# Optimization experiments

Hardware: AMD Instinct MI355X
Metric: run time of the kernel (lower is better)

The kernel has to match this reference:

```python
import jax, jax.numpy as jnp
import numpy as np
import math

D_MODEL = 512
N_HEADS = 8
D_FF = 2048
TOP_FACTOR = 5
LN_EPS = 1e-5


def _layernorm(x, g, b):
    m = jnp.mean(x, axis=-1, keepdims=True)
    v = jnp.mean((x - m) ** 2, axis=-1, keepdims=True)
    return (x - m) / jnp.sqrt(v + LN_EPS) * g + b


def _prob_sparse_attn(q_in, k_in, v_in, wq, bq, wk, bk, wv, bv, wo, bo):
    # weights stored (in, out): y = x @ w + b  (equivalent to torch Linear)
    B, Lq, dm = q_in.shape
    Lk = k_in.shape[1]
    H, D = N_HEADS, dm // N_HEADS
    q = (q_in @ wq + bq).reshape(B, Lq, H, D).transpose(0, 2, 1, 3)  # (B,H,Lq,D)
    k = (k_in @ wk + bk).reshape(B, Lk, H, D).transpose(0, 2, 1, 3)
    v = (v_in @ wv + bv).reshape(B, Lk, H, D).transpose(0, 2, 1, 3)

    qn = q / jnp.linalg.norm(q, axis=-1, keepdims=True)
    kn = k / jnp.linalg.norm(k, axis=-1, keepdims=True)
    # full cosine-similarity matrix, reduced to a row mean (as in the original)
    scores_all = jnp.einsum('bhqd,bhkd->bhqk', qn, kn)
    mean_scores = scores_all.mean(axis=-1)  # (B,H,Lq)

    u = max(1, Lq // TOP_FACTOR)
    _, top_idx = jax.lax.top_k(mean_scores, u)  # (B,H,u)

    q_sel = jnp.take_along_axis(q, top_idx[..., None], axis=2)  # (B,H,u,D)
    scores = jnp.einsum('bhud,bhkd->bhuk', q_sel, k) / math.sqrt(D)
    attn = jax.nn.softmax(scores, axis=-1)
    ctx_sel = jnp.einsum('bhuk,bhkd->bhud', attn, v)  # (B,H,u,D)

    b_ix = jnp.arange(B)[:, None, None]
    h_ix = jnp.arange(H)[None, :, None]
    context = jnp.zeros((B, H, Lq, D), dtype=q.dtype).at[b_ix, h_ix, top_idx].set(ctx_sel)
    out = context.transpose(0, 2, 1, 3).reshape(B, Lq, dm)
    return out @ wo + bo


def _decoder_layer(x, enc_out, p):
    xn = _layernorm(x, p['ln1_g'], p['ln1_b'])
    x = x + _prob_sparse_attn(xn, xn, xn, p['sa_wq'], p['sa_bq'], p['sa_wk'], p['sa_bk'],
                              p['sa_wv'], p['sa_bv'], p['sa_wo'], p['sa_bo'])
    xn = _layernorm(x, p['ln2_g'], p['ln2_b'])
    x = x + _prob_sparse_attn(xn, enc_out, enc_out, p['ca_wq'], p['ca_bq'], p['ca_wk'], p['ca_bk'],
                              p['ca_wv'], p['ca_bv'], p['ca_wo'], p['ca_bo'])
    xn = _layernorm(x, p['ln3_g'], p['ln3_b'])
    h = jax.nn.relu(xn @ p['ff_w1'] + p['ff_b1'])
    return x + (h @ p['ff_w2'] + p['ff_b2'])


def setup_inputs() -> dict:
    key = jax.random.key(0)
    ks = iter(jax.random.split(key, 32))
    B, L = 2, 2048
    dm, dff = D_MODEL, D_FF
    s = 1.0 / math.sqrt(dm)
    inp = {
        'x': jax.random.normal(next(ks), (B, L, dm), jnp.float32),
        'enc_out': jax.random.normal(next(ks), (B, L, dm), jnp.float32),
    }
    for pre in ('sa', 'ca'):
        for nm in ('wq', 'wk', 'wv', 'wo'):
            inp[f'{pre}_{nm}'] = jax.random.normal(next(ks), (dm, dm), jnp.float32) * s
            inp[f'{pre}_{nm[1:] and "b" + nm[1:]}'] = jnp.zeros((dm,), jnp.float32)
    inp['ff_w1'] = jax.random.normal(next(ks), (dm, dff), jnp.float32) * s
    inp['ff_b1'] = jnp.zeros((dff,), jnp.float32)
    inp['ff_w2'] = jax.random.normal(next(ks), (dff, dm), jnp.float32) / math.sqrt(dff)
    inp['ff_b2'] = jnp.zeros((dm,), jnp.float32)
    for i in (1, 2, 3):
        inp[f'ln{i}_g'] = jnp.ones((dm,), jnp.float32)
        inp[f'ln{i}_b'] = jnp.zeros((dm,), jnp.float32)
    return inp


def reference(x, enc_out,
              sa_wq, sa_bq, sa_wk, sa_bk, sa_wv, sa_bv, sa_wo, sa_bo,
              ca_wq, ca_bq, ca_wk, ca_bk, ca_wv, ca_bv, ca_wo, ca_bo,
              ff_w1, ff_b1, ff_w2, ff_b2,
              ln1_g, ln1_b, ln2_g, ln2_b, ln3_g, ln3_b):
    p = dict(sa_wq=sa_wq, sa_bq=sa_bq, sa_wk=sa_wk, sa_bk=sa_bk, sa_wv=sa_wv, sa_bv=sa_bv,
             sa_wo=sa_wo, sa_bo=sa_bo, ca_wq=ca_wq, ca_bq=ca_bq, ca_wk=ca_wk, ca_bk=ca_bk,
             ca_wv=ca_wv, ca_bv=ca_bv, ca_wo=ca_wo, ca_bo=ca_bo,
             ff_w1=ff_w1, ff_b1=ff_b1, ff_w2=ff_w2, ff_b2=ff_b2,
             ln1_g=ln1_g, ln1_b=ln1_b, ln2_g=ln2_g, ln2_b=ln2_b, ln3_g=ln3_g, ln3_b=ln3_b)
    return _decoder_layer(x, enc_out, p)
```

## Files before the change

### kernel.cpp

```cpp
#include <hip/hip_runtime.h>

#define BB 2
#define LL 2048
#define DM 512
#define NH 8
#define DH 64
#define DFF 2048
#define UU 409
#define ROWS (BB*LL)
#define X_ELEMS 2097152
#define NCHUNK 8

typedef unsigned short u16;
typedef __attribute__((ext_vector_type(8))) short short8;
typedef __attribute__((ext_vector_type(4))) float floatx4;

#define G_TOTAL 38200000
__device__ float g_buf[G_TOTAL];
__device__ int   g_isbf16;

#define A_Q     10495488
#define A_K     12592640
#define A_V     14689792
#define A_MKN   25175552
#define A_MS    25176576
#define A_RANK  25209344
#define A_PARTK 25242112
#define A_LIST  25274880
#define A_PO    25281536
#define A_PML   29475840
#define A_CTXF  16786944
#define XN_H    16796672
#define XN_L    18893824
#define CTX_H   33573888
#define CTX_L   35671040
#define ENC_H   37768192
#define ENC_L   39865344
#define AH_H    41962496
#define KH16    59213824
#define KL16    61310976
#define VTH16   63408128
#define VTL16   65505280
#define WT_SAQKV 67864576
#define WT_SAO   69437440
#define WT_CAQ   69961728
#define WT_CAKV  70486016
#define WT_CAO   71534592
#define WT_W1    72058880
#define WT_W2    74156032

__constant__ int c_end[28] = {
    2097152, 4194304, 4456448, 4456960, 4719104, 4719616, 4981760, 4982272,
    5244416, 5244928, 5507072, 5507584, 5769728, 5770240, 6032384, 6032896,
    6295040, 6295552, 7344128, 7346176, 8394752, 8395264, 8395776, 8396288,
    8396800, 8397312, 8397824, 8398336
};
__constant__ int sm_idx[16] = {3,5,7,9,11,13,15,17,19,21,22,23,24,25,26,27};
__constant__ int sm_cum[16] = {64,128,192,256,320,384,448,512,768,832,896,960,1024,1088,1152,1216};
#define XG 262144
#define EG 262144
#define SG 1216

__device__ __forceinline__ float bf2f(u16 x) {
    union { unsigned int u; float f; } c; c.u = ((unsigned int)x) << 16; return c.f;
}
__device__ __forceinline__ u16 f2bf(float f) {
    union { float f; unsigned int u; } c; c.f = f;
    unsigned int u = c.u;
    return (u16)((u + 0x7FFFu + ((u >> 16) & 1u)) >> 16);
}
__device__ __forceinline__ unsigned cvtpk_bf16(float a, float b) {
    unsigned r;
    asm("v_cvt_pk_bf16_f32 %0, %1, %2" : "=v"(r) : "v"(a), "v"(b));
    return r;
}

struct P28 { const void* p[28]; };
struct I3 { int v[3]; };

__constant__ int tj[10][6] = {
    {2,  WT_SAQKV, 0,    512,  786432, 8},
    {4,  WT_SAQKV, 512,  512,  786432, 8},
    {6,  WT_SAQKV, 1024, 512,  786432, 8},
    {8,  WT_SAO,   0,    512,  262144, 8},
    {10, WT_CAQ,   0,    512,  262144, 8},
    {12, WT_CAKV,  0,    512,  524288, 8},
    {14, WT_CAKV,  512,  512,  524288, 8},
    {16, WT_CAO,   0,    512,  262144, 8},
    {18, WT_W1,    0,    512, 1048576, 32},
    {20, WT_W2,    0,   2048, 1048576, 8},
};
__constant__ int tcum[10] = {64, 128, 192, 256, 320, 384, 448, 512, 768, 1024};
__global__ void prep_all(P28 ps) {
    const int f = (((const u16*)ps.p[22])[0] == 0x3F80u) ? 1 : 0;
    if (blockIdx.x == 0 && threadIdx.x == 0) g_isbf16 = f;
    u16* gb16 = (u16*)g_buf;
    if (blockIdx.x < 1024) {
        int bid = blockIdx.x;
        int j = 0;
        while (bid >= tcum[j]) j++;
        int t = bid - (j ? tcum[j - 1] : 0);
        int widx = tj[j][0], wt = tj[j][1], col0 = tj[j][2];
        int K = tj[j][3], lo = tj[j][4], txn = tj[j][5];
        int Nsrc = txn * 64;
        int n0 = (t % txn) * 64, k0 = (t / txn) * 64;
        __shared__ float tb[64][65];
        int c = threadIdx.x & 63, r0 = threadIdx.x >> 6;
        const void* W = ps.p[widx];
        u16* WTh = gb16 + wt;
        for (int i = 0; i < 16; i++) {
            int r = r0 + 4 * i;
            size_t src = (size_t)(k0 + r) * Nsrc + n0 + c;
            tb[r][c] = f ? bf2f(((const u16*)W)[src]) : ((const float*)W)[src];
        }
        __syncthreads();
        for (int i = 0; i < 16; i++) {
            int r = r0 + 4 * i;
            float v = tb[c][r];
            u16 hi = f2bf(v);
            size_t o = (size_t)(col0 + n0 + r) * K + k0 + c;
            WTh[o] = hi;
            WTh[lo + o] = f2bf(v - bf2f(hi));
        }
        return;
    }
    int stride = 2048 * blockDim.x;
    for (int g = (blockIdx.x - 1024) * blockDim.x + threadIdx.x; g < XG + EG + SG; g += stride) {
        if (g < XG) {
            int e = g * 8;
            if (f) {
                uint4 raw = ((const uint4*)ps.p[0])[g];
                const u16* rr = (const u16*)&raw;
                float v[8] __attribute__((aligned(16)));
#pragma unroll
                for (int i = 0; i < 8; i++) v[i] = bf2f(rr[i]);
                *(float4*)(g_buf + e) = ((const float4*)v)[0];
                *(float4*)(g_buf + e + 4) = ((const float4*)v)[1];
            } else {
                *(uint4*)(g_buf + e)     = ((const uint4*)ps.p[0])[g * 2];
                *(uint4*)(g_buf + e + 4) = ((const uint4*)ps.p[0])[g * 2 + 1];
            }
        } else if (g < XG + EG) {
            int gl = g - XG;
            int e = gl * 8;
            float v[8] __attribute__((aligned(16)));
            if (f) {
                uint4 raw = ((const uint4*)ps.p[1])[gl];
                const u16* rr = (const u16*)&raw;
#pragma unroll
                for (int i = 0; i < 8; i++) v[i] = bf2f(rr[i]);
            } else {
                *(float4*)(v)     = ((const float4*)ps.p[1])[gl * 2];
                *(float4*)(v + 4) = ((const float4*)ps.p[1])[gl * 2 + 1];
            }
            u16 hh[8] __attribute__((aligned(16)));
            u16 lo[8] __attribute__((aligned(16)));
#pragma unroll
            for (int i = 0; i < 8; i++) { u16 hi = f2bf(v[i]); hh[i] = hi; lo[i] = f2bf(v[i] - bf2f(hi)); }
            *(uint4*)(&gb16[ENC_H + e]) = *(const uint4*)hh;
            *(uint4*)(&gb16[ENC_L + e]) = *(const uint4*)lo;
        } else {
            int t = g - XG - EG;
            int si = 0;
            while (t >= sm_cum[si]) si++;
            int s = sm_idx[si];
            int gl = t - (si ? sm_cum[si - 1] : 0);
            int e = gl * 8;
            float* dst = g_buf + c_end[s - 1] + e;
            if (f) {
                uint4 raw = *(const uint4*)((const u16*)ps.p[s] + e);
                const u16* rr = (const u16*)&raw;
#pragma unroll
                for (int i = 0; i < 8; i++) dst[i] = bf2f(rr[i]);
            } else {
                *(uint4*)(dst)     = *(const uint4*)((const float*)ps.p[s] + e);
                *(uint4*)(dst + 4) = *(const uint4*)((const float*)ps.p[s] + e + 4);
            }
        }
    }
}

__global__ void lnorm_k(int x_off, int g_off, int b_off, int yh_u16, int yl_u16) {
    int row = blockIdx.x;
    int tid = threadIdx.x;
    const float* x = g_buf + x_off + (size_t)row * DM;
    float a = x[tid], c = x[tid + 256];
    float s1 = a + c, s2 = a * a + c * c;
    for (int o = 32; o > 0; o >>= 1) { s1 += __shfl_xor(s1, o); s2 += __shfl_xor(s2, o); }
    __shared__ float r1[4], r2[4];
    int wave = tid >> 6, lane = tid & 63;
    if (lane == 0) { r1[wave] = s1; r2[wave] = s2; }
    __syncthreads();
    s1 = r1[0] + r1[1] + r1[2] + r1[3];
    s2 = r2[0] + r2[1] + r2[2] + r2[3];
    float mean = s1 * (1.0f / DM);
    float var  = s2 * (1.0f / DM) - mean * mean;
    float rstd = rsqrtf(var + 1e-5f);
    const float* gg = g_buf + g_off;
    const float* bb = g_buf + b_off;
    u16* yh = ((u16*)g_buf) + yh_u16 + (size_t)row * DM;
    u16* yl = ((u16*)g_buf) + yl_u16 + (size_t)row * DM;
    float v1 = (a - mean) * rstd * gg[tid]       + bb[tid];
    float v2 = (c - mean) * rstd * gg[tid + 256] + bb[tid + 256];
    u16 h1 = f2bf(v1), h2 = f2bf(v2);
    yh[tid] = h1;       yl[tid] = f2bf(v1 - bf2f(h1));
    yh[tid + 256] = h2; yl[tid + 256] = f2bf(v2 - bf2f(h2));
}

template<int WM, bool SPLIT, bool SEC, bool RELU, bool RESID, bool FINAL, bool OUTH>
__global__ void mgemm_k(I3 a_offs, I3 splt, I3 alz, int wt_u16_off, I3 boffs, int resid_off,
                        int out_off, void* __restrict__ dext, int M, int N, int K) {
    constexpr int BT_M = WM * 32;
    constexpr int A4 = BT_M * 4;
    __shared__ u16 Ash[BT_M * 40];
    __shared__ u16 Asl[SPLIT ? BT_M * 40 : 8];
    __shared__ u16 Bsh[128 * 40];
    __shared__ u16 Bsl[SPLIT ? 128 * 40 : 8];
    int sec_blk = SEC ? ((blockIdx.x * 128) >> 9) : 0;
    const u16* Ah = ((const u16*)g_buf) + a_offs.v[sec_blk];
    const u16* Al = Ah + (size_t)M * K;
    const u16* WTh = ((const u16*)g_buf) + wt_u16_off;
    const u16* WTl = WTh + (size_t)N * K;
    const int isbf = g_isbf16;
    const bool use_al = SPLIT && splt.v[sec_blk] && !(alz.v[sec_blk] && isbf);
    const bool use_bl = SPLIT && splt.v[sec_blk] && !isbf;
    int tid = threadIdx.x;
    int lane = tid & 63, wid = tid >> 6;
    int wm = wid >> 1, wn = wid & 1;
    int quad = lane >> 4, l15 = lane & 15;
    int m0 = blockIdx.y * BT_M, n0 = blockIdx.x * 128;
    floatx4 acc[WM][4];
#pragma unroll
    for (int i = 0; i < WM; i++)
#pragma unroll
        for (int j = 0; j < 4; j++) acc[i][j] = (floatx4){0.f, 0.f, 0.f, 0.f};
    for (int k0 = 0; k0 < K; k0 += 32) {
#pragma unroll
        for (int i = 0; i < (A4 + 255) / 256; i++) {
            int idx8 = tid + 256 * i;
            if (A4 % 256 == 0 || idx8 < A4) {
                int r = idx8 >> 2, c8 = (idx8 & 3) * 8;
                *(uint4*)(&Ash[r * 40 + c8]) = *(const uint4*)(Ah + (size_t)(m0 + r) * K + k0 + c8);
                if (SPLIT && use_al)
                    *(uint4*)(&Asl[r * 40 + c8]) = *(const uint4*)(Al + (size_t)(m0 + r) * K + k0 + c8);
            }
        }
#pragma unroll
        for (int i = 0; i < 2; i++) {
            int idx8 = tid + 256 * i;
            int r = idx8 >> 2, c8 = (idx8 & 3) * 8;
            *(uint4*)(&Bsh[r * 40 + c8]) = *(const uint4*)(WTh + (size_t)(n0 + r) * K + k0 + c8);
            if (SPLIT && use_bl)
                *(uint4*)(&Bsl[r * 40 + c8]) = *(const uint4*)(WTl + (size_t)(n0 + r) * K + k0 + c8);
        }
        __syncthreads();
        short8 ah[WM], bh[4], al[WM], bl[4];
#pragma unroll
        for (int i = 0; i < WM; i++) {
            int ro = (wm * WM * 16 + i * 16 + l15) * 40 + quad * 8;
            ah[i] = *(const short8*)(&Ash[ro]);
            if (SPLIT && use_al) al[i] = *(const short8*)(&Asl[ro]);
        }
#pragma unroll
        for (int j = 0; j < 4; j++) {
            int ro = (wn * 64 + j * 16 + l15) * 40 + quad * 8;
            bh[j] = *(const short8*)(&Bsh[ro]);
            if (SPLIT && use_bl) bl[j] = *(const short8*)(&Bsl[ro]);
        }
#pragma unroll
        for (int i = 0; i < WM; i++)
#pragma unroll
            for (int j = 0; j < 4; j++) {
                acc[i][j] = __builtin_amdgcn_mfma_f32_16x16x32_bf16(ah[i], bh[j], acc[i][j], 0, 0, 0);
                if constexpr (SPLIT) {
                    if (use_bl)
                        acc[i][j] = __builtin_amdgcn_mfma_f32_16x16x32_bf16(ah[i], bl[j], acc[i][j], 0, 0, 0);
                    if (use_al)
                        acc[i][j] = __builtin_amdgcn_mfma_f32_16x16x32_bf16(al[i], bh[j], acc[i][j], 0, 0, 0);
                }
            }
        __syncthreads();
    }
#pragma unroll
    for (int i = 0; i < WM; i++)
#pragma unroll
        for (int j = 0; j < 4; j++)
#pragma unroll
            for (int r = 0; r < 4; r++) {
                int row = m0 + wm * WM * 16 + i * 16 + quad * 4 + r;
                int col = n0 + wn * 64 + j * 16 + l15;
                int sec = SEC ? (col >> 9) : 0;
                int ci  = SEC ? (col & 511) : col;
                float v = acc[i][j][r] + g_buf[boffs.v[sec] + ci];
                if (RELU) v = fmaxf(v, 0.f);
                if (RESID) v += g_buf[resid_off + (size_t)row * N + col];
                if (FINAL) {
                    if (g_isbf16) ((u16*)dext)[(size_t)row * N + col] = f2bf(v);
                    else          ((float*)dext)[(size_t)row * N + col] = v;
                } else if (OUTH) {
                    ((u16*)g_buf)[out_off + (size_t)row * N + col] = f2bf(v);
                } else if (SEC) {
                    g_buf[out_off + ((size_t)sec * ROWS + row) * 512 + ci] = v;
                } else {
                    g_buf[out_off + (size_t)row * N + col] = v;
                }
            }
}

template<bool SPLIT, bool RESID, bool FINAL>
__global__ __launch_bounds__(64, 2) void sgemm_k(int a_off, int sp, int alz, int wt_u16_off,
        int b_off, int resid_off, int out_off, void* __restrict__ dext, int M, int N, int K) {
    const u16* gb = (const u16*)g_buf;
    const u16* Ah = gb + a_off;
    const u16* Alp = Ah + (size_t)M * K;
    const u16* Bh = gb + wt_u16_off;
    const u16* Blp = Bh + (size_t)N * K;
    const int isbf = g_isbf16;
    const bool ual = SPLIT && sp && !(alz && isbf);
    const bool ubl = SPLIT && sp && !isbf;
    int ntiles = N >> 6;
    int bid = blockIdx.x;
    int nt = bid % ntiles, mt = bid / ntiles;
    int n0 = nt * 64, m0 = mt * 16;
    int lane = threadIdx.x;
    int quad = lane >> 4, l15 = lane & 15;
    const u16* ap  = Ah  + (size_t)(m0 + l15) * K + quad * 8;
    const u16* alq = Alp + (size_t)(m0 + l15) * K + quad * 8;
    const u16* bp  = Bh  + (size_t)(n0 + l15) * K + quad * 8;
    const u16* blq = Blp + (size_t)(n0 + l15) * K + quad * 8;
    floatx4 acc[4];
#pragma unroll
    for (int j = 0; j < 4; j++) acc[j] = (floatx4){0.f, 0.f, 0.f, 0.f};
#pragma unroll 2
    for (int k0 = 0; k0 < K; k0 += 32) {
        short8 ah = *(const short8*)(ap + k0);
        short8 al;
        if (ual) al = *(const short8*)(alq + k0);
        short8 bh[4], bl[4];
#pragma unroll
        for (int j = 0; j < 4; j++) {
            bh[j] = *(const short8*)(bp + (size_t)j * 16 * K + k0);
            if (ubl) bl[j] = *(const short8*)(blq + (size_t)j * 16 * K + k0);
        }
#pragma unroll
        for (int j = 0; j < 4; j++) {
            acc[j] = __builtin_amdgcn_mfma_f32_16x16x32_bf16(ah, bh[j], acc[j], 0, 0, 0);
            if constexpr (SPLIT) {
                if (ubl) acc[j] = __builtin_amdgcn_mfma_f32_16x16x32_bf16(ah, bl[j], acc[j], 0, 0, 0);
                if (ual) acc[j] = __builtin_amdgcn_mfma_f32_16x16x32_bf16(al, bh[j], acc[j], 0, 0, 0);
            }
        }
    }
    const float* bias = g_buf + b_off;
#pragma unroll
    for (int j = 0; j < 4; j++)
#pragma unroll
        for (int r = 0; r < 4; r++) {
            int row = m0 + quad * 4 + r;
            int col = n0 + j * 16 + l15;
            float v = acc[j][r] + bias[col];
            if (RESID) v += g_buf[resid_off + (size_t)row * N + col];
            if (FINAL) {
                if (isbf) ((u16*)dext)[(size_t)row * N + col] = f2bf(v);
                else      ((float*)dext)[(size_t)row * N + col] = v;
            } else {
                g_buf[out_off + (size_t)row * N + col] = v;
            }
        }
}

__global__ void meankn_p1(int k_off, int part_off) {
    int bh = blockIdx.x >> 5, chunk = blockIdx.x & 31;
    int b = bh >> 3, h = bh & 7;
    int wave = threadIdx.x >> 6, lane = threadIdx.x & 63;
    const float* base = g_buf + k_off + (size_t)b * LL * DM + (size_t)h * DH + lane;
    float acc = 0.f;
    for (int t = 0; t < 16; t++) {
        int j = chunk * 64 + wave * 16 + t;
        float kv = base[(size_t)j * DM];
        float s = kv * kv;
        for (int o = 32; o > 0; o >>= 1) s += __shfl_xor(s, o);
        acc += kv / sqrtf(fmaxf(s, 1e-30f));
    }
    __shared__ float red[4][64];
    red[wave][lane] = acc;
    __syncthreads();
    if (threadIdx.x < 64)
        g_buf[part_off + (size_t)blockIdx.x * 64 + threadIdx.x] =
            red[0][threadIdx.x] + red[1][threadIdx.x] + red[2][threadIdx.x] + red[3][threadIdx.x];
}

__global__ void mscore_k(int q_off, int part_off, int ms_off) {
    int bh = blockIdx.y, b = bh >> 3, h = bh & 7;
    int tid = threadIdx.x;
    __shared__ float mk[64];
    if (tid < 64) {
        float s = 0.f;
        for (int c = 0; c < 32; c++) s += g_buf[part_off + (size_t)(bh * 32 + c) * 64 + tid];
        mk[tid] = s * (1.0f / LL);
    }
    __syncthreads();
    int w = tid >> 6, lane = tid & 63;
    float m = mk[lane];
#pragma unroll
    for (int it = 0; it < 8; it++) {
        int row = blockIdx.x * 32 + it * 4 + w;
        float qv = g_buf[q_off + ((size_t)b * LL + row) * DM + h * DH + lane];
        float s = qv * qv, d = qv * m;
        for (int o = 32; o > 0; o >>= 1) { s += __shfl_xor(s, o); d += __shfl_xor(d, o); }
        if (lane == 0) g_buf[ms_off + bh * LL + row] = d / sqrtf(fmaxf(s, 1e-30f));
    }
}

__global__ void topsel_k(int ms_off, int list_off, int rank_off, int u) {
    __shared__ float s[LL];
    int bh = blockIdx.y, chunk = blockIdx.x;
    for (int i = threadIdx.x; i < LL; i += 256) s[i] = g_buf[ms_off + bh * LL + i];
    __syncthreads();
    int il = threadIdx.x >> 2;
    int i = chunk * 64 + il;
    int jq = threadIdx.x & 3;
    float si = s[i];
    int cnt = 0;
    for (int t = 0; t < 512; t++) {
        int j = jq * 512 + t;
        float sj = s[j];
        cnt += (sj > si) || (sj == si && j < i);
    }
    cnt += __shfl_xor(cnt, 1);
    cnt += __shfl_xor(cnt, 2);
    if (jq == 0) {
        int* list = (int*)(g_buf + list_off);
        int* rank = (int*)(g_buf + rank_off);
        if (cnt < u) { list[bh * 416 + cnt] = i; rank[bh * LL + i] = cnt; }
        else rank[bh * LL + i] = -1;
    }
}

template<bool LO>
__global__ void kvprep_k(int k_off, int v_off) {
    int bh = blockIdx.y, b = bh >> 3, h = bh & 7;
    int tok0 = blockIdx.x * 64;
    int tid = threadIdx.x;
    __shared__ float vt[64][68];
    u16* gb16 = (u16*)g_buf;
    int tok = tid >> 2, dq = (tid & 3) * 16;
    const float* kp = g_buf + k_off + ((size_t)(b * LL + tok0 + tok)) * DM + h * DH + dq;
    const float* vp = g_buf + v_off + ((size_t)(b * LL + tok0 + tok)) * DM + h * DH + dq;
    float kv[16] __attribute__((aligned(16)));
#pragma unroll
    for (int i = 0; i < 4; i++) *(float4*)(kv + 4 * i) = *(const float4*)(kp + 4 * i);
    u16 hh[16] __attribute__((aligned(16)));
    u16 lo[16] __attribute__((aligned(16)));
#pragma unroll
    for (int i = 0; i < 16; i++) { hh[i] = f2bf(kv[i]); if (LO) lo[i] = f2bf(kv[i] - bf2f(hh[i])); }
    size_t ko = ((size_t)(bh * LL + tok0 + tok)) * DH + dq;
    *(uint4*)(gb16 + KH16 + ko)     = ((const uint4*)hh)[0];
    *(uint4*)(gb16 + KH16 + ko + 8) = ((const uint4*)hh)[1];
    if (LO) {
        *(uint4*)(gb16 + KL16 + ko)     = ((const uint4*)lo)[0];
        *(uint4*)(gb16 + KL16 + ko + 8) = ((const uint4*)lo)[1];
    }
#pragma unroll
    for (int i = 0; i < 4; i++) *(float4*)(&vt[tok][dq + 4 * i]) = *(const float4*)(vp + 4 * i);
    __syncthreads();
    int d = tid >> 2, tq = (tid & 3) * 16;
    float vv[16];
#pragma unroll
    for (int i = 0; i < 16; i++) vv[i] = vt[tq + i][d];
#pragma unroll
    for (int i = 0; i < 16; i++) { hh[i] = f2bf(vv[i]); if (LO) lo[i] = f2bf(vv[i] - bf2f(hh[i])); }
    size_t vo = ((size_t)(bh * DH + d)) * LL + tok0 + tq;
    *(uint4*)(gb16 + VTH16 + vo)     = ((const uint4*)hh)[0];
    *(uint4*)(gb16 + VTH16 + vo + 8) = ((const uint4*)hh)[1];
    if (LO) {
        *(uint4*)(gb16 + VTL16 + vo)     = ((const uint4*)lo)[0];
        *(uint4*)(gb16 + VTL16 + vo + 8) = ((const uint4*)lo)[1];
    }
}

template<bool S3>
__global__ __launch_bounds__(256, 4) void attn_flash(int q_off, int kh_off, int kl_off,
        int vth_off, int vtl_off, int list_off, int po_off, int pml_off, int u) {
    int bid = blockIdx.x;
    int grp = bid & 127;
    int sxt = bid >> 7;
    int bh = grp & 15, chunk = grp >> 4;
    int b = bh >> 3, h = bh & 7;
    int tid = threadIdx.x, lane = tid & 63, w = tid >> 6;
    int quad = lane >> 4, l15 = lane & 15;
    const int* list = (const int*)(g_buf + list_off);

    short8 qh[2], ql[2];
    {
        int slot_q = sxt * 64 + w * 16 + l15;
        int qidx = list[bh * 416 + (slot_q < u ? slot_q : u - 1)];
        const float* qp = g_buf + q_off + ((size_t)b * LL + qidx) * DM + h * DH;
#pragma unroll
        for (int d2 = 0; d2 < 2; d2++) {
            float v[8] __attribute__((aligned(16)));
            *(float4*)(v)     = *(const float4*)(qp + d2 * 32 + quad * 8);
            *(float4*)(v + 4) = *(const float4*)(qp + d2 * 32 + quad * 8 + 4);
            u16 hh[8] __attribute__((aligned(16)));
            u16 lo[8] __attribute__((aligned(16)));
#pragma unroll
            for (int j = 0; j < 8; j++) {
                float s = v[j] * 0.125f;
                u16 hi = f2bf(s); hh[j] = hi; lo[j] = f2bf(s - bf2f(hi));
            }
            qh[d2] = *(const short8*)hh; ql[d2] = *(const short8*)lo;
        }
    }

    __shared__ u16 Ksh[32 * 68];
    __shared__ u16 Ksl[S3 ? 32 * 68 : 8];
    __shared__ u16 Vth[64 * 36];
    __shared__ u16 Vtl[S3 ? 64 * 36 : 8];

    const u16* gb16 = (const u16*)g_buf;
    const u16* KHp = gb16 + kh_off + (size_t)bh * LL * DH;
    const u16* KLp = gb16 + kl_off + (size_t)bh * LL * DH;
    const u16* VHp = gb16 + vth_off + (size_t)bh * DH * LL;
    const u16* VLp = gb16 + vtl_off + (size_t)bh * DH * LL;
    int krow = tid >> 3, kcol = (tid & 7) * 8;
    int vd = tid >> 2, vcol = (tid & 3) * 8;

    int aA = ((((lane >> 4) & 1) << 5) | l15) << 2;
    int aB = aA + 64;
    bool hiT = (quad >= 2);

    uint4 pre[S3 ? 4 : 2];
    auto issue = [&](int row0) {
        pre[0] = *(const uint4*)(KHp + (size_t)(row0 + krow) * DH + kcol);
        pre[1] = *(const uint4*)(VHp + (size_t)vd * LL + row0 + vcol);
        if constexpr (S3) {
            pre[2] = *(const uint4*)(KLp + (size_t)(row0 + krow) * DH + kcol);
            pre[3] = *(const uint4*)(VLp + (size_t)vd * LL + row0 + vcol);
        }
    };
    auto commit = [&]() {
        *(uint4*)(&Ksh[krow * 68 + kcol]) = pre[0];
        *(uint4*)(&Vth[vd * 36 + vcol]) = pre[1];
        if constexpr (S3) {
            *(uint4*)(&Ksl[krow * 68 + kcol]) = pre[2];
            *(uint4*)(&Vtl[vd * 36 + vcol]) = pre[3];
        }
    };

    float m_run = -3.0e38f, l_run = 0.f;
    floatx4 acc_o[4];
#pragma unroll
    for (int j = 0; j < 4; j++) acc_o[j] = (floatx4){0.f, 0.f, 0.f, 0.f};

    issue(chunk * 256);
    for (int kt = 0; kt < 8; ++kt) {
        __syncthreads();
        commit();
        if (kt < 7) issue(chunk * 256 + (kt + 1) * 32);
        __syncthreads();
        floatx4 sacc[2];
#pragma unroll
        for (int t = 0; t < 2; t++) {
            sacc[t] = (floatx4){0.f, 0.f, 0.f, 0.f};
#pragma unroll
            for (int d2 = 0; d2 < 2; d2++) {
                int ro = (t * 16 + l15) * 68 + d2 * 32 + quad * 8;
                short8 kh = *(const short8*)(&Ksh[ro]);
                sacc[t] = __builtin_amdgcn_mfma_f32_16x16x32_bf16(kh, qh[d2], sacc[t], 0, 0, 0);
                sacc[t] = __builtin_amdgcn_mfma_f32_16x16x32_bf16(kh, ql[d2], sacc[t], 0, 0, 0);
                if constexpr (S3) {
                    short8 kl = *(const short8*)(&Ksl[ro]);
                    sacc[t] = __builtin_amdgcn_mfma_f32_16x16x32_bf16(kl, qh[d2], sacc[t], 0, 0, 0);
                }
            }
        }
        float mx = fmaxf(fmaxf(fmaxf(sacc[0][0], sacc[0][1]), fmaxf(sacc[0][2], sacc[0][3])),
                         fmaxf(fmaxf(sacc[1][0], sacc[1][1]), fmaxf(sacc[1][2], sacc[1][3])));
        mx = fmaxf(mx, __shfl_xor(mx, 16));
        mx = fmaxf(mx, __shfl_xor(mx, 32));
        float mn = fmaxf(m_run, mx);
        float alpha = __expf(m_run - mn);
        m_run = mn;
#pragma unroll
        for (int t = 0; t < 2; t++)
#pragma unroll
            for (int r = 0; r < 4; r++) sacc[t][r] = __expf(sacc[t][r] - mn);
        float ls = (sacc[0][0] + sacc[0][1]) + (sacc[0][2] + sacc[0][3])
                 + (sacc[1][0] + sacc[1][1]) + (sacc[1][2] + sacc[1][3]);
        ls += __shfl_xor(ls, 16);
        ls += __shfl_xor(ls, 32);
        l_run = l_run * alpha + ls;
        unsigned phw[2][2], plw[2][2];
#pragma unroll
        for (int t = 0; t < 2; t++)
#pragma unroll
            for (int hh = 0; hh < 2; hh++) {
                float s0 = sacc[t][2 * hh], s1 = sacc[t][2 * hh + 1];
                unsigned hw = cvtpk_bf16(s0, s1);
                phw[t][hh] = hw;
                float r0 = s0 - __uint_as_float(hw << 16);
                float r1 = s1 - __uint_as_float(hw & 0xFFFF0000u);
                plw[t][hh] = cvtpk_bf16(r0, r1);
            }
        union { unsigned wd[4]; short8 v; } pbh, pbl;
#pragma unroll
        for (int hh = 0; hh < 2; hh++) {
            int a0 = __builtin_amdgcn_ds_bpermute(aA, (int)phw[0][hh]);
            int a1 = __builtin_amdgcn_ds_bpermute(aA, (int)phw[1][hh]);
            pbh.wd[hh] = (unsigned)(hiT ? a1 : a0);
            int b0 = __builtin_amdgcn_ds_bpermute(aB, (int)phw[0][hh]);
            int b1 = __builtin_amdgcn_ds_bpermute(aB, (int)phw[1][hh]);
            pbh.wd[2 + hh] = (unsigned)(hiT ? b1 : b0);
            int c0 = __builtin_amdgcn_ds_bpermute(aA, (int)plw[0][hh]);
            int c1 = __builtin_amdgcn_ds_bpermute(aA, (int)plw[1][hh]);
            pbl.wd[hh] = (unsigned)(hiT ? c1 : c0);
            int d0 = __builtin_amdgcn_ds_bpermute(aB, (int)plw[0][hh]);
            int d1 = __builtin_amdgcn_ds_bpermute(aB, (int)plw[1][hh]);
            pbl.wd[2 + hh] = (unsigned)(hiT ? d1 : d0);
        }
#pragma unroll
        for (int j = 0; j < 4; j++)
#pragma unroll
            for (int r = 0; r < 4; r++) acc_o[j][r] *= alpha;
#pragma unroll
        for (int j = 0; j < 4; j++) {
            int ro = (j * 16 + l15) * 36 + quad * 8;
            short8 vh = *(const short8*)(&Vth[ro]);
            acc_o[j] = __builtin_amdgcn_mfma_f32_16x16x32_bf16(vh, pbh.v, acc_o[j], 0, 0, 0);
            acc_o[j] = __builtin_amdgcn_mfma_f32_16x16x32_bf16(vh, pbl.v, acc_o[j], 0, 0, 0);
            if constexpr (S3) {
                short8 vl = *(const short8*)(&Vtl[ro]);
                acc_o[j] = __builtin_amdgcn_mfma_f32_16x16x32_bf16(vl, pbh.v, acc_o[j], 0, 0, 0);
            }
        }
    }
    int slot = sxt * 64 + w * 16 + l15;
    if (slot < u) {
        size_t rec = ((size_t)(bh * NCHUNK + chunk)) * 512 + slot;
        float* po = g_buf + po_off + rec * 64;
#pragma unroll
        for (int j = 0; j < 4; j++)
            *(float4*)(po + j * 16 + quad * 4) = *(const float4*)&acc_o[j];
        if (quad == 0) {
            float* pml = g_buf + pml_off + rec * 2;
            pml[0] = m_run; pml[1] = l_run;
        }
    }
}

__global__ void attn_combine(int po_off, int pml_off, int rank_off, int u) {
    int bh = blockIdx.y;
    int b = bh >> 3, h = bh & 7;
    int tid = threadIdx.x;
    int qi = tid >> 4;
    int kb = tid & 15;
    int ds = kb * 4;
    int row = blockIdx.x * 16 + qi;
    int rank = ((const int*)(g_buf + rank_off))[bh * LL + row];
    size_t idx = ((size_t)b * LL + row) * DM + h * DH + ds;
    if (rank < 0) {
        ushort4 z = {0, 0, 0, 0};
        *(ushort4*)(((u16*)g_buf) + CTX_H + idx) = z;
        *(ushort4*)(((u16*)g_buf) + CTX_L + idx) = z;
        return;
    }
    float m = -3.0e38f;
#pragma unroll
    for (int c = 0; c < NCHUNK; c++)
        m = fmaxf(m, g_buf[pml_off + (((size_t)(bh * NCHUNK + c)) * 512 + rank) * 2]);
    float l = 0.f, O0 = 0.f, O1 = 0.f, O2 = 0.f, O3 = 0.f;
#pragma unroll
    for (int c = 0; c < NCHUNK; c++) {
        size_t rec = ((size_t)(bh * NCHUNK + c)) * 512 + rank;
        const float* pml = g_buf + pml_off + rec * 2;
        float a = __expf(pml[0] - m);
        l += a * pml[1];
        float4 o = *(const float4*)(g_buf + po_off + rec * 64 + ds);
        O0 += a * o.x; O1 += a * o.y; O2 += a * o.z; O3 += a * o.w;
    }
    float inv = 1.0f / l;
    float o0 = O0 * inv, o1 = O1 * inv, o2 = O2 * inv, o3 = O3 * inv;
    ushort4 hv, lv;
    hv.x = f2bf(o0); lv.x = f2bf(o0 - bf2f(hv.x));
    hv.y = f2bf(o1); lv.y = f2bf(o1 - bf2f(hv.y));
    hv.z = f2bf(o2); lv.z = f2bf(o2 - bf2f(hv.z));
    hv.w = f2bf(o3); lv.w = f2bf(o3 - bf2f(hv.w));
    *(ushort4*)(((u16*)g_buf) + CTX_H + idx) = hv;
    *(ushort4*)(((u16*)g_buf) + CTX_L + idx) = lv;
}

extern "C" void kernel_launch(void* const* d_in, const int* in_sizes, int n_in,
                              void* d_out, int out_size, void* d_ws, size_t ws_size,
                              hipStream_t stream) {
    static const int SZ[28] = {
        2097152, 2097152,
        262144, 512, 262144, 512, 262144, 512, 262144, 512,
        262144, 512, 262144, 512, 262144, 512, 262144, 512,
        1048576, 2048, 1048576, 512,
        512, 512, 512, 512, 512, 512
    };
    int OFF[28];
    int cur = 0;
    for (int i = 0; i < 28; i++) { OFF[i] = cur; cur += SZ[i]; }

    P28 ps;
    for (int i = 0; i < 28; i++) ps.p[i] = d_in[i];
    prep_all<<<3072, 256, 0, stream>>>(ps);

    auto select_attend = [&](bool sa) {
        if (sa) kvprep_k<true><<<dim3(32, 16), 256, 0, stream>>>(A_K, A_V);
        else    kvprep_k<false><<<dim3(32, 16), 256, 0, stream>>>(A_K, A_V);
        meankn_p1<<<16 * 32, 256, 0, stream>>>(A_K, A_PARTK);
        mscore_k<<<dim3(64, 16), 256, 0, stream>>>(A_Q, A_PARTK, A_MS);
        topsel_k<<<dim3(32, 16), 256, 0, stream>>>(A_MS, A_LIST, A_RANK, UU);
        if (sa)
            attn_flash<true><<<896, 256, 0, stream>>>(
                A_Q, KH16, KL16, VTH16, VTL16, A_LIST, A_PO, A_PML, UU);
        else
            attn_flash<false><<<896, 256, 0, stream>>>(
                A_Q, KH16, KL16, VTH16, VTL16, A_LIST, A_PO, A_PML, UU);
        attn_combine<<<dim3(128, 16), 256, 0, stream>>>(A_PO, A_PML, A_RANK, UU);
    };

    lnorm_k<<<ROWS, 256, 0, stream>>>(OFF[0], OFF[22], OFF[23], XN_H, XN_L);
    mgemm_k<2, true, true, false, false, false, false><<<dim3(12, 64), 256, 0, stream>>>(
        I3{{XN_H, XN_H, XN_H}}, I3{{1, 1, 1}}, I3{{0, 0, 0}},
        WT_SAQKV, I3{{OFF[3], OFF[5], OFF[7]}}, 0, A_Q, nullptr, ROWS, 1536, 512);
    select_attend(true);
    sgemm_k<true, true, false><<<2048, 64, 0, stream>>>(
        CTX_H, 1, 0, WT_SAO, OFF[9], OFF[0], OFF[0], nullptr, ROWS, 512, 512);

    lnorm_k<<<ROWS, 256, 0, stream>>>(OFF[0], OFF[24], OFF[25], XN_H, XN_L);
    sgemm_k<true, false, false><<<2048, 64, 0, stream>>>(
        XN_H, 1, 0, WT_CAQ, OFF[11], 0, A_Q, nullptr, ROWS, 512, 512);
    mgemm_k<2, true, true, false, false, false, false><<<dim3(8, 64), 256, 0, stream>>>(
        I3{{ENC_H, ENC_H, ENC_H}}, I3{{1, 0, 0}}, I3{{1, 0, 0}},
        WT_CAKV, I3{{OFF[13], OFF[15], 0}}, 0, A_K, nullptr, ROWS, 1024, 512);
    select_attend(false);
    sgemm_k<false, true, false><<<2048, 64, 0, stream>>>(
        CTX_H, 0, 0, WT_CAO, OFF[17], OFF[0], OFF[0], nullptr, ROWS, 512, 512);

    lnorm_k<<<ROWS, 256, 0, stream>>>(OFF[0], OFF[26], OFF[27], XN_H, XN_L);
    mgemm_k<4, false, false, true, false, false, true><<<dim3(16, 32), 256, 0, stream>>>(
        I3{{XN_H, 0, 0}}, I3{{0, 0, 0}}, I3{{0, 0, 0}},
        WT_W1, I3{{OFF[19], 0, 0}}, 0, AH_H, nullptr, ROWS, 2048, 512);
    sgemm_k<false, true, true><<<2048, 64, 0, stream>>>(
        AH_H, 0, 0, WT_W2, OFF[21], OFF[0], 0, d_out, ROWS, 512, 2048);
}
```

Baseline: 623.2 us.

## Prefetch next k-slice in sgemm and swap block order to M-fastest in GEMMs

The skinny GEMM kernel now double-buffers its register fragments, loading the next k-step's A/B fragments before issuing the MFMAs for the current one, so global-load latency can overlap with compute. It also drops the min-blocks-per-CU launch bound, which gives the compiler more registers for the extra buffers. Both GEMM kernels switch block rasterization so consecutive blocks walk M with a fixed N tile, aiming for better weight-tile reuse in cache. The costs are higher register pressure and possibly fewer waves resident per CU.

```diff
diff --git a/kernel.cpp b/kernel.cpp
--- a/kernel.cpp
+++ b/kernel.cpp
@@ -216,7 +216,8 @@
     __shared__ u16 Asl[SPLIT ? BT_M * 40 : 8];
     __shared__ u16 Bsh[128 * 40];
     __shared__ u16 Bsl[SPLIT ? 128 * 40 : 8];
-    int sec_blk = SEC ? ((blockIdx.x * 128) >> 9) : 0;
+    int ntb = blockIdx.y;
+    int sec_blk = SEC ? ((ntb * 128) >> 9) : 0;
     const u16* Ah = ((const u16*)g_buf) + a_offs.v[sec_blk];
     const u16* Al = Ah + (size_t)M * K;
     const u16* WTh = ((const u16*)g_buf) + wt_u16_off;
@@ -228,7 +229,7 @@
     int lane = tid & 63, wid = tid >> 6;
     int wm = wid >> 1, wn = wid & 1;
     int quad = lane >> 4, l15 = lane & 15;
-    int m0 = blockIdx.y * BT_M, n0 = blockIdx.x * 128;
+    int m0 = blockIdx.x * BT_M, n0 = ntb * 128;
     floatx4 acc[WM][4];
 #pragma unroll
     for (int i = 0; i < WM; i++)
@@ -308,7 +309,7 @@
 }
 
 template<bool SPLIT, bool RESID, bool FINAL>
-__global__ __launch_bounds__(64, 2) void sgemm_k(int a_off, int sp, int alz, int wt_u16_off,
+__global__ __launch_bounds__(64) void sgemm_k(int a_off, int sp, int alz, int wt_u16_off,
         int b_off, int resid_off, int out_off, void* __restrict__ dext, int M, int N, int K) {
     const u16* gb = (const u16*)g_buf;
     const u16* Ah = gb + a_off;
@@ -318,9 +319,9 @@
     const int isbf = g_isbf16;
     const bool ual = SPLIT && sp && !(alz && isbf);
     const bool ubl = SPLIT && sp && !isbf;
-    int ntiles = N >> 6;
+    int mtiles = M >> 4;
     int bid = blockIdx.x;
-    int nt = bid % ntiles, mt = bid / ntiles;
+    int mt = bid % mtiles, nt = bid / mtiles;
     int n0 = nt * 64, m0 = mt * 16;
     int lane = threadIdx.x;
     int quad = lane >> 4, l15 = lane & 15;
@@ -331,24 +332,40 @@
     floatx4 acc[4];
 #pragma unroll
     for (int j = 0; j < 4; j++) acc[j] = (floatx4){0.f, 0.f, 0.f, 0.f};
-#pragma unroll 2
+    short8 ah_c, al_c, bh_c[4], bl_c[4];
+    ah_c = *(const short8*)(ap);
+    if (ual) al_c = *(const short8*)(alq);
+#pragma unroll
+    for (int j = 0; j < 4; j++) {
+        bh_c[j] = *(const short8*)(bp + (size_t)j * 16 * K);
+        if (ubl) bl_c[j] = *(const short8*)(blq + (size_t)j * 16 * K);
+    }
     for (int k0 = 0; k0 < K; k0 += 32) {
-        short8 ah = *(const short8*)(ap + k0);
-        short8 al;
-        if (ual) al = *(const short8*)(alq + k0);
-        short8 bh[4], bl[4];
+        short8 ah_n, al_n, bh_n[4], bl_n[4];
+        int kn = k0 + 32;
+        if (kn < K) {
+            ah_n = *(const short8*)(ap + kn);
+            if (ual) al_n = *(const short8*)(alq + kn);
+#pragma unroll
+            for (int j = 0; j < 4; j++) {
+                bh_n[j] = *(const short8*)(bp + (size_t)j * 16 * K + kn);
+                if (ubl) bl_n[j] = *(const short8*)(blq + (size_t)j * 16 * K + kn);
+            }
+        }
 #pragma unroll
         for (int j = 0; j < 4; j++) {
-            bh[j] = *(const short8*)(bp + (size_t)j * 16 * K + k0);
-            if (ubl) bl[j] = *(const short8*)(blq + (size_t)j * 16 * K + k0);
-        }
+            acc[j] = __builtin_amdgcn_mfma_f32_16x16x32_bf16(ah_c, bh_c[j], acc[j], 0, 0, 0);
+            if constexpr (SPLIT) {
+                if (ubl) acc[j] = __builtin_amdgcn_mfma_f32_16x16x32_bf16(ah_c, bl_c[j], acc[j], 0, 0, 0);
+                if (ual) acc[j] = __builtin_amdgcn_mfma_f32_16x16x32_bf16(al_c, bh_c[j], acc[j], 0, 0, 0);
+            }
+        }
+        ah_c = ah_n;
+        if (ual) al_c = al_n;
 #pragma unroll
         for (int j = 0; j < 4; j++) {
-            acc[j] = __builtin_amdgcn_mfma_f32_16x16x32_bf16(ah, bh[j], acc[j], 0, 0, 0);
-            if constexpr (SPLIT) {
-                if (ubl) acc[j] = __builtin_amdgcn_mfma_f32_16x16x32_bf16(ah, bl[j], acc[j], 0, 0, 0);
-                if (ual) acc[j] = __builtin_amdgcn_mfma_f32_16x16x32_bf16(al, bh[j], acc[j], 0, 0, 0);
-            }
+            bh_c[j] = bh_n[j];
+            if (ubl) bl_c[j] = bl_n[j];
         }
     }
     const float* bias = g_buf + b_off;
@@ -723,7 +740,7 @@
     };
 
     lnorm_k<<<ROWS, 256, 0, stream>>>(OFF[0], OFF[22], OFF[23], XN_H, XN_L);
-    mgemm_k<2, true, true, false, false, false, false><<<dim3(12, 64), 256, 0, stream>>>(
+    mgemm_k<2, true, true, false, false, false, false><<<dim3(64, 12), 256, 0, stream>>>(
         I3{{XN_H, XN_H, XN_H}}, I3{{1, 1, 1}}, I3{{0, 0, 0}},
         WT_SAQKV, I3{{OFF[3], OFF[5], OFF[7]}}, 0, A_Q, nullptr, ROWS, 1536, 512);
     select_attend(true);
@@ -733,7 +750,7 @@
     lnorm_k<<<ROWS, 256, 0, stream>>>(OFF[0], OFF[24], OFF[25], XN_H, XN_L);
     sgemm_k<true, false, false><<<2048, 64, 0, stream>>>(
         XN_H, 1, 0, WT_CAQ, OFF[11], 0, A_Q, nullptr, ROWS, 512, 512);
-    mgemm_k<2, true, true, false, false, false, false><<<dim3(8, 64), 256, 0, stream>>>(
+    mgemm_k<2, true, true, false, false, false, false><<<dim3(64, 8), 256, 0, stream>>>(
         I3{{ENC_H, ENC_H, ENC_H}}, I3{{1, 0, 0}}, I3{{1, 0, 0}},
         WT_CAKV, I3{{OFF[13], OFF[15], 0}}, 0, A_K, nullptr, ROWS, 1024, 512);
     select_attend(false);
@@ -741,7 +758,7 @@
         CTX_H, 0, 0, WT_CAO, OFF[17], OFF[0], OFF[0], nullptr, ROWS, 512, 512);
 
     lnorm_k<<<ROWS, 256, 0, stream>>>(OFF[0], OFF[26], OFF[27], XN_H, XN_L);
-    mgemm_k<4, false, false, true, false, false, true><<<dim3(16, 32), 256, 0, stream>>>(
+    mgemm_k<4, false, false, true, false, false, true><<<dim3(32, 16), 256, 0, stream>>>(
         I3{{XN_H, 0, 0}}, I3{{0, 0, 0}}, I3{{0, 0, 0}},
         WT_W1, I3{{OFF[19], 0, 0}}, 0, AH_H, nullptr, ROWS, 2048, 512);
     sgemm_k<false, true, true><<<2048, 64, 0, stream>>>(
```

After: 601.9 us. 1.04x faster.
